# Kernel tuning notes

Measured on AMD Instinct MI355X. Metric: run time of the kernel, lower is better.

Reference implementation:

```python
import jax, jax.numpy as jnp
import numpy as np

H = 28
W = 28
CIN = 128
COUT = 32
K = 3
SHIFT = 1  # fixed shift_direction (original draws +/-1 at init)


def setup_inputs() -> dict:
    key = jax.random.key(0)
    kx, kw = jax.random.split(key)
    x = jax.random.normal(kx, (512, CIN, H, W), dtype=jnp.float32)
    w = jax.random.normal(kw, (COUT, CIN, K), dtype=jnp.float32)
    return {"x": x, "w": w}


def reference(x, w):
    # Original: reshape to (B, C*H, W, 1), unfold with kernel (3,1) pad (1,0)
    # -> conv with kernel 3 along the W axis, then einsum contracts channel
    # and kernel dims (128->32), then roll by +1 along H.
    B = x.shape[0]
    xp = jnp.pad(x, ((0, 0), (0, 0), (0, 0), (1, 1)))  # pad W by 1 each side
    # windows: (B, CIN, H, K, W) — mirrors the unfold+reshape to (1,128,28,3,28)
    win = jnp.stack([xp[..., k:k + W] for k in range(K)], axis=3)
    # einsum 'limkn, jik -> ljmn' with batch dim: contract channel i and tap k
    y = jnp.einsum('bihkn,jik->bjhn', win, w)  # (B, COUT, H, W)
    # permute->(B,H,COUT,W), roll along H, permute back == roll on axis 2 here
    y = jnp.roll(y, SHIFT, axis=2)
    return y
```

## Files before the change

kernel.cpp:

```cpp
#include <hip/hip_runtime.h>
#include <hip/hip_bf16.h>

#define CIN_  128
#define H_    28
#define W_    28
#define COUT_ 32
#define B_    512

typedef __attribute__((ext_vector_type(8))) short short8;
typedef __attribute__((ext_vector_type(4))) float f32x4;

__device__ __forceinline__ unsigned short f2bfu(float f) {
    union { __hip_bfloat16 h; unsigned short s; } u;
    u.h = __float2bfloat16(f);
    return u.s;
}
__device__ __forceinline__ short f2bf(float f) { return (short)f2bfu(f); }

__global__ void prep_w_kernel(const float* __restrict__ w, short* __restrict__ wsA) {
    int t = blockIdx.x * 256 + threadIdx.x;
    int frag = t >> 9;
    int rem  = t & 511;
    int l = rem >> 3;
    int j = rem & 7;
    int mt = frag / 12;
    int kc = frag % 12;
    int tap = kc >> 2;
    int i  = (kc & 3) * 32 + (l >> 4) * 8 + j;
    int jo = mt * 16 + (l & 15);
    wsA[t] = f2bf(w[(jo * CIN_ + i) * 3 + tap]);
}

template<bool USE_WS>
__global__ __launch_bounds__(256, 5)
void conv_kernel(const float* __restrict__ x, const float* __restrict__ w,
                 const short* __restrict__ wsA, float* __restrict__ out) {
    __shared__ short lds[4][30 * CIN_];
    const int tid = threadIdx.x;
    const int wv  = tid >> 6;
    const int l   = tid & 63;
    const int hg  = blockIdx.x;
    const int b   = blockIdx.y;
    const int h0  = hg * 4;

    const float* xb = x + (size_t)b * (CIN_ * H_ * W_);

    {
        int s   = (tid & 63) * 4;
        int row = (s >= 128) ? 29 : 0;
        int c   = s & 127;
        *reinterpret_cast<ulong1*>(&lds[wv][row * CIN_ + c]) = ulong1{0};
    }

    f32x4 v0[7], v1[7];
#pragma unroll
    for (int it = 0; it < 7; ++it) {
        int f4 = it * 256 + tid;
        int c  = f4 / 28;
        int q  = f4 % 28;
        const float* p = xb + (2 * c) * (H_ * W_) + h0 * W_ + q * 4;
        v0[it] = *reinterpret_cast<const f32x4*>(p);
        v1[it] = *reinterpret_cast<const f32x4*>(p + H_ * W_);
    }

#pragma unroll
    for (int it = 0; it < 7; ++it) {
        int f4 = it * 256 + tid;
        int c  = f4 / 28;
        int q  = f4 % 28;
        int hl = q / 7;
        int w4 = q % 7;
        int* buf = reinterpret_cast<int*>(&lds[hl][0]);
#pragma unroll
        for (int e = 0; e < 4; ++e) {
            int wt  = w4 * 4 + e + 1;
            int idx = wt * 64 + ((((c >> 2) ^ (wt & 15) ^ hl) << 2) | (c & 3));
            unsigned word = (unsigned)f2bfu(v0[it][e]) |
                            ((unsigned)f2bfu(v1[it][e]) << 16);
            buf[idx] = (int)word;
        }
    }

    short8 a0[6], a1[6];
    if (USE_WS) {
#pragma unroll
        for (int k6 = 0; k6 < 6; ++k6) {
            a0[k6] = *reinterpret_cast<const short8*>(wsA + k6 * 512 + l * 8);
            a1[k6] = *reinterpret_cast<const short8*>(wsA + (12 + k6) * 512 + l * 8);
        }
    } else {
#pragma unroll
        for (int k6 = 0; k6 < 6; ++k6) {
            int tap = k6 >> 2;
            int ib  = (k6 & 3) * 32 + (l >> 4) * 8;
#pragma unroll
            for (int j = 0; j < 8; ++j) {
                a0[k6][j] = f2bf(w[((l & 15) * CIN_ + ib + j) * 3 + tap]);
                a1[k6][j] = f2bf(w[((16 + (l & 15)) * CIN_ + ib + j) * 3 + tap]);
            }
        }
    }
    __syncthreads();

    short* wbuf = lds[wv];
    const int h  = h0 + wv;
    const int ho = (h + 1 == H_) ? 0 : (h + 1);
    float* ob = out + (size_t)b * (COUT_ * H_ * W_) + ho * W_;

#pragma unroll
    for (int nt = 0; nt < 2; ++nt) {
        f32x4 acc0, acc1;
#pragma unroll
        for (int q = 0; q < 4; ++q) { acc0[q] = 0.0f; acc1[q] = 0.0f; }

#pragma unroll
        for (int half = 0; half < 2; ++half) {
            if (nt + half > 0) {
                if (USE_WS) {
#pragma unroll
                    for (int k6 = 0; k6 < 6; ++k6) {
                        int kc = half * 6 + k6;
                        a0[k6] = *reinterpret_cast<const short8*>(wsA + kc * 512 + l * 8);
                        a1[k6] = *reinterpret_cast<const short8*>(wsA + (12 + kc) * 512 + l * 8);
                    }
                } else {
#pragma unroll
                    for (int k6 = 0; k6 < 6; ++k6) {
                        int kc  = half * 6 + k6;
                        int tap = kc >> 2;
                        int ib  = (kc & 3) * 32 + (l >> 4) * 8;
#pragma unroll
                        for (int j = 0; j < 8; ++j) {
                            a0[k6][j] = f2bf(w[((l & 15) * CIN_ + ib + j) * 3 + tap]);
                            a1[k6][j] = f2bf(w[((16 + (l & 15)) * CIN_ + ib + j) * 3 + tap]);
                        }
                    }
                }
            }
#pragma unroll
            for (int k6 = 0; k6 < 6; ++k6) {
                int kc  = half * 6 + k6;
                int tap = kc >> 2;
                int cch = (kc & 3) * 4 + (l >> 4);
                int wt  = nt * 16 + (l & 15) + tap;
                int wtc = wt > 29 ? 29 : wt;
                const short8 bfrag = *reinterpret_cast<const short8*>(
                    &wbuf[wtc * CIN_ + ((cch ^ (wtc & 15) ^ wv) << 3)]);
                acc0 = __builtin_amdgcn_mfma_f32_16x16x32_bf16(a0[k6], bfrag, acc0, 0, 0, 0);
                acc1 = __builtin_amdgcn_mfma_f32_16x16x32_bf16(a1[k6], bfrag, acc1, 0, 0, 0);
            }
        }

        {
            int wcol = nt * 16 + (l & 15);
            if (wcol < W_) {
                int jb = (l >> 4) * 4;
#pragma unroll
                for (int rr = 0; rr < 4; ++rr) {
                    ob[(jb + rr) * (H_ * W_) + wcol]        = acc0[rr];
                    ob[(16 + jb + rr) * (H_ * W_) + wcol]   = acc1[rr];
                }
            }
        }
    }
}

extern "C" void kernel_launch(void* const* d_in, const int* in_sizes, int n_in,
                              void* d_out, int out_size, void* d_ws, size_t ws_size,
                              hipStream_t stream) {
    (void)in_sizes; (void)n_in; (void)out_size;
    const float* x = (const float*)d_in[0];
    const float* w = (const float*)d_in[1];
    float* out = (float*)d_out;

    if (ws_size >= (size_t)(24 * 512 * sizeof(short))) {
        short* wsA = (short*)d_ws;
        prep_w_kernel<<<dim3(48), dim3(256), 0, stream>>>(w, wsA);
        conv_kernel<true><<<dim3(7, 512), dim3(256), 0, stream>>>(x, w, wsA, out);
    } else {
        conv_kernel<false><<<dim3(7, 512), dim3(256), 0, stream>>>(x, w, (const short*)nullptr, out);
    }
}
```

Measured before the change: 64.45 us.

## Make conv blocks persistent per batch with double-buffered row-pair pipeline

Result: slower. 105.3 us (+63.4%).

```diff
diff --git a/kernel.cpp b/kernel.cpp
--- a/kernel.cpp
+++ b/kernel.cpp
@@ -32,133 +32,136 @@
 }
 
 template<bool USE_WS>
-__global__ __launch_bounds__(256, 5)
+__global__ __launch_bounds__(256, 3)
 void conv_kernel(const float* __restrict__ x, const float* __restrict__ w,
                  const short* __restrict__ wsA, float* __restrict__ out) {
     __shared__ short lds[4][30 * CIN_];
     const int tid = threadIdx.x;
     const int wv  = tid >> 6;
     const int l   = tid & 63;
-    const int hg  = blockIdx.x;
-    const int b   = blockIdx.y;
-    const int h0  = hg * 4;
+    const int r   = wv >> 1;
+    const int mt  = wv & 1;
+    const int b   = blockIdx.x;
 
     const float* xb = x + (size_t)b * (CIN_ * H_ * W_);
+    float*       ob = out + (size_t)b * (COUT_ * H_ * W_);
 
     {
-        int s   = (tid & 63) * 4;
-        int row = (s >= 128) ? 29 : 0;
-        int c   = s & 127;
-        *reinterpret_cast<ulong1*>(&lds[wv][row * CIN_ + c]) = ulong1{0};
+        int idx = tid * 2;
+        int bi  = idx >> 7;
+        int wrd = idx & 127;
+        int row = (wrd >> 6) ? 29 : 0;
+        int ci  = wrd & 63;
+        *reinterpret_cast<ulong1*>(
+            reinterpret_cast<int*>(&lds[bi][0]) + row * 64 + ci) = ulong1{0};
     }
 
-    f32x4 v0[7], v1[7];
+    f32x4 v0[4], v1[4];
 #pragma unroll
-    for (int it = 0; it < 7; ++it) {
-        int f4 = it * 256 + tid;
-        int c  = f4 / 28;
-        int q  = f4 % 28;
-        const float* p = xb + (2 * c) * (H_ * W_) + h0 * W_ + q * 4;
-        v0[it] = *reinterpret_cast<const f32x4*>(p);
-        v1[it] = *reinterpret_cast<const f32x4*>(p + H_ * W_);
-    }
-
-#pragma unroll
-    for (int it = 0; it < 7; ++it) {
-        int f4 = it * 256 + tid;
-        int c  = f4 / 28;
-        int q  = f4 % 28;
-        int hl = q / 7;
-        int w4 = q % 7;
-        int* buf = reinterpret_cast<int*>(&lds[hl][0]);
-#pragma unroll
-        for (int e = 0; e < 4; ++e) {
-            int wt  = w4 * 4 + e + 1;
-            int idx = wt * 64 + ((((c >> 2) ^ (wt & 15) ^ hl) << 2) | (c & 3));
-            unsigned word = (unsigned)f2bfu(v0[it][e]) |
-                            ((unsigned)f2bfu(v1[it][e]) << 16);
-            buf[idx] = (int)word;
+    for (int it = 0; it < 4; ++it) {
+        int s = it * 256 + tid;
+        if (s < 896) {
+            int c = s / 14, q = s % 14;
+            int hl = q / 7, w4 = q % 7;
+            const float* p = xb + (2 * c) * (H_ * W_) + hl * W_ + w4 * 4;
+            v0[it] = *reinterpret_cast<const f32x4*>(p);
+            v1[it] = *reinterpret_cast<const f32x4*>(p + H_ * W_);
         }
     }
 
-    short8 a0[6], a1[6];
+    short8 af[12];
     if (USE_WS) {
 #pragma unroll
-        for (int k6 = 0; k6 < 6; ++k6) {
-            a0[k6] = *reinterpret_cast<const short8*>(wsA + k6 * 512 + l * 8);
-            a1[k6] = *reinterpret_cast<const short8*>(wsA + (12 + k6) * 512 + l * 8);
-        }
+        for (int kc = 0; kc < 12; ++kc)
+            af[kc] = *reinterpret_cast<const short8*>(wsA + (mt * 12 + kc) * 512 + l * 8);
     } else {
 #pragma unroll
-        for (int k6 = 0; k6 < 6; ++k6) {
-            int tap = k6 >> 2;
-            int ib  = (k6 & 3) * 32 + (l >> 4) * 8;
+        for (int kc = 0; kc < 12; ++kc) {
+            int tap = kc >> 2;
+            int ib  = (kc & 3) * 32 + (l >> 4) * 8;
 #pragma unroll
-            for (int j = 0; j < 8; ++j) {
-                a0[k6][j] = f2bf(w[((l & 15) * CIN_ + ib + j) * 3 + tap]);
-                a1[k6][j] = f2bf(w[((16 + (l & 15)) * CIN_ + ib + j) * 3 + tap]);
+            for (int j = 0; j < 8; ++j)
+                af[kc][j] = f2bf(w[((mt * 16 + (l & 15)) * CIN_ + ib + j) * 3 + tap]);
+        }
+    }
+
+#pragma unroll 2
+    for (int g = 0; g < 14; ++g) {
+        const int par = g & 1;
+
+#pragma unroll
+        for (int it = 0; it < 4; ++it) {
+            int s = it * 256 + tid;
+            if (s < 896) {
+                int c = s / 14, q = s % 14;
+                int hl = q / 7, w4 = q % 7;
+                int bi = par * 2 + hl;
+                int* buf = reinterpret_cast<int*>(&lds[bi][0]);
+#pragma unroll
+                for (int e = 0; e < 4; ++e) {
+                    int wt  = w4 * 4 + e + 1;
+                    int idx = wt * 64 + (((((c >> 2) ^ (wt & 15) ^ bi) & 15) << 2) | (c & 3));
+                    unsigned word = (unsigned)f2bfu(v0[it][e]) |
+                                    ((unsigned)f2bfu(v1[it][e]) << 16);
+                    buf[idx] = (int)word;
+                }
             }
         }
-    }
-    __syncthreads();
 
-    short* wbuf = lds[wv];
-    const int h  = h0 + wv;
-    const int ho = (h + 1 == H_) ? 0 : (h + 1);
-    float* ob = out + (size_t)b * (COUT_ * H_ * W_) + ho * W_;
+        if (g < 13) {
+            const int h0n = (g + 1) * 2;
+#pragma unroll
+            for (int it = 0; it < 4; ++it) {
+                int s = it * 256 + tid;
+                if (s < 896) {
+                    int c = s / 14, q = s % 14;
+                    int hl = q / 7, w4 = q % 7;
+                    const float* p = xb + (2 * c) * (H_ * W_) + (h0n + hl) * W_ + w4 * 4;
+                    v0[it] = *reinterpret_cast<const f32x4*>(p);
+                    v1[it] = *reinterpret_cast<const f32x4*>(p + H_ * W_);
+                }
+            }
+            __builtin_amdgcn_sched_barrier(0);
+        }
+
+        asm volatile("s_waitcnt lgkmcnt(0)" ::: "memory");
+        __builtin_amdgcn_sched_barrier(0);
+        __builtin_amdgcn_s_barrier();
+        __builtin_amdgcn_sched_barrier(0);
+
+        const int bi = par * 2 + r;
+        short* wbuf = &lds[bi][0];
+        f32x4 acc[2];
+#pragma unroll
+        for (int q = 0; q < 4; ++q) { acc[0][q] = 0.0f; acc[1][q] = 0.0f; }
 
 #pragma unroll
-    for (int nt = 0; nt < 2; ++nt) {
-        f32x4 acc0, acc1;
+        for (int kc = 0; kc < 12; ++kc) {
+            int tap = kc >> 2;
+            int cch = (kc & 3) * 4 + (l >> 4);
 #pragma unroll
-        for (int q = 0; q < 4; ++q) { acc0[q] = 0.0f; acc1[q] = 0.0f; }
-
-#pragma unroll
-        for (int half = 0; half < 2; ++half) {
-            if (nt + half > 0) {
-                if (USE_WS) {
-#pragma unroll
-                    for (int k6 = 0; k6 < 6; ++k6) {
-                        int kc = half * 6 + k6;
-                        a0[k6] = *reinterpret_cast<const short8*>(wsA + kc * 512 + l * 8);
-                        a1[k6] = *reinterpret_cast<const short8*>(wsA + (12 + kc) * 512 + l * 8);
-                    }
-                } else {
-#pragma unroll
-                    for (int k6 = 0; k6 < 6; ++k6) {
-                        int kc  = half * 6 + k6;
-                        int tap = kc >> 2;
-                        int ib  = (kc & 3) * 32 + (l >> 4) * 8;
-#pragma unroll
-                        for (int j = 0; j < 8; ++j) {
-                            a0[k6][j] = f2bf(w[((l & 15) * CIN_ + ib + j) * 3 + tap]);
-                            a1[k6][j] = f2bf(w[((16 + (l & 15)) * CIN_ + ib + j) * 3 + tap]);
-                        }
-                    }
-                }
-            }
-#pragma unroll
-            for (int k6 = 0; k6 < 6; ++k6) {
-                int kc  = half * 6 + k6;
-                int tap = kc >> 2;
-                int cch = (kc & 3) * 4 + (l >> 4);
+            for (int nt = 0; nt < 2; ++nt) {
                 int wt  = nt * 16 + (l & 15) + tap;
                 int wtc = wt > 29 ? 29 : wt;
                 const short8 bfrag = *reinterpret_cast<const short8*>(
-                    &wbuf[wtc * CIN_ + ((cch ^ (wtc & 15) ^ wv) << 3)]);
-                acc0 = __builtin_amdgcn_mfma_f32_16x16x32_bf16(a0[k6], bfrag, acc0, 0, 0, 0);
-                acc1 = __builtin_amdgcn_mfma_f32_16x16x32_bf16(a1[k6], bfrag, acc1, 0, 0, 0);
+                    &wbuf[wtc * CIN_ + ((((cch ^ (wtc & 15) ^ bi) & 15)) << 3)]);
+                acc[nt] = __builtin_amdgcn_mfma_f32_16x16x32_bf16(
+                    af[kc], bfrag, acc[nt], 0, 0, 0);
             }
         }
 
         {
-            int wcol = nt * 16 + (l & 15);
-            if (wcol < W_) {
-                int jb = (l >> 4) * 4;
+            const int h  = g * 2 + r;
+            const int ho = (h + 1 == H_) ? 0 : (h + 1);
 #pragma unroll
-                for (int rr = 0; rr < 4; ++rr) {
-                    ob[(jb + rr) * (H_ * W_) + wcol]        = acc0[rr];
-                    ob[(16 + jb + rr) * (H_ * W_) + wcol]   = acc1[rr];
+            for (int nt = 0; nt < 2; ++nt) {
+                int wcol = nt * 16 + (l & 15);
+                if (wcol < W_) {
+#pragma unroll
+                    for (int rr = 0; rr < 4; ++rr) {
+                        int j = mt * 16 + (l >> 4) * 4 + rr;
+                        ob[(j * H_ + ho) * W_ + wcol] = acc[nt][rr];
+                    }
                 }
             }
         }
@@ -176,8 +179,8 @@
     if (ws_size >= (size_t)(24 * 512 * sizeof(short))) {
         short* wsA = (short*)d_ws;
         prep_w_kernel<<<dim3(48), dim3(256), 0, stream>>>(w, wsA);
-        conv_kernel<true><<<dim3(7, 512), dim3(256), 0, stream>>>(x, w, wsA, out);
+        conv_kernel<true><<<dim3(B_), dim3(256), 0, stream>>>(x, w, wsA, out);
     } else {
-        conv_kernel<false><<<dim3(7, 512), dim3(256), 0, stream>>>(x, w, (const short*)nullptr, out);
+        conv_kernel<false><<<dim3(B_), dim3(256), 0, stream>>>(x, w, (const short*)nullptr, out);
     }
 }
```
